# Performance work log

Measured on AMD Instinct MI355X. Metric: run time of the kernel, lower is better.

Reference implementation:

```python
import jax, jax.numpy as jnp
import numpy as np

T, N, E, D, H = 128, 1024, 16384, 256, 8


def setup_inputs() -> dict:
    key = jax.random.key(0)
    ks = jax.random.split(key, 8)
    s = 0.02  # weight init scale
    return {
        "embeddings": jax.random.normal(ks[0], (T, N, D), jnp.float32),
        "W1": jax.random.normal(ks[1], (D, 2 * D), jnp.float32) * s,
        "b1": jnp.zeros((2 * D,), jnp.float32),
        "W2": jax.random.normal(ks[2], (2 * D, D), jnp.float32) * s,
        "b2": jnp.zeros((D,), jnp.float32),
        "Wq": jax.random.normal(ks[3], (D, D), jnp.float32) * s,
        "bq": jnp.zeros((D,), jnp.float32),
        "Wk": jax.random.normal(ks[4], (D, D), jnp.float32) * s,
        "bk": jnp.zeros((D,), jnp.float32),
        "edge_val": jax.random.uniform(ks[5], (T, E), jnp.float32),
        "edge_src": jax.random.randint(ks[6], (T, E), 0, N),
        "edge_dst": jax.random.randint(ks[7], (T, E), 0, N),
    }


def _pos_encoding(t, d):
    # sin/cos interleaved positional encoding, pe[:,0::2]=sin, pe[:,1::2]=cos
    pos = jnp.arange(t, dtype=jnp.float32)[:, None]
    div = jnp.exp(jnp.arange(0, d, 2, dtype=jnp.float32) * (-np.log(10000.0) / d))
    ang = pos * div  # [t, d//2]
    return jnp.stack([jnp.sin(ang), jnp.cos(ang)], axis=-1).reshape(t, d)


def reference(embeddings, W1, b1, W2, b2, Wq, bq, Wk, bk, edge_val, edge_src, edge_dst):
    t, n, d = embeddings.shape
    hd = d // H
    # per-timestep node MLP + avg/max pooling over nodes  -> one vector per snapshot
    h = jax.nn.relu(embeddings @ W1 + b1)          # [T, N, 2D]
    pooled = h.mean(axis=1) + h.max(axis=1)        # [T, 2D] (adaptive avg+max pool to 1)
    x = jax.nn.relu(pooled @ W2 + b2)              # [T, D]
    x = x + _pos_encoding(t, d)
    # multi-head self-attention probabilities (batch=1), averaged over heads
    q = ((x @ Wq + bq) * (hd ** -0.5)).reshape(t, H, hd)
    k = (x @ Wk + bk).reshape(t, H, hd)
    scores = jnp.einsum('qhd,khd->hqk', q, k)      # [H, T, T]
    probs = jax.nn.softmax(scores, axis=-1).mean(axis=0)  # [T, T]
    # threshold, add identity, causal (lower-triangular) mask
    probs = jnp.where(probs < 1.0 / t, 0.0, probs)
    probs = (probs + jnp.eye(t, dtype=probs.dtype)) * jnp.tril(jnp.ones((t, t), probs.dtype))
    # build adjacency stack from edge lists (COO scatter), then weighted accumulation
    t_idx = jnp.arange(t)[:, None]
    A = jnp.zeros((t, n, n), embeddings.dtype).at[t_idx, edge_src, edge_dst].add(edge_val)
    # new_At[t] = sum_s probs[t, s] * A[s]
    return jnp.einsum('ts,snm->tnm', probs, A)
```

## Files before the change

kernel.cpp:

```cpp
#include <hip/hip_runtime.h>
#include <hip/hip_bf16.h>

#define T_ 128
#define N_ 1024
#define E_ 16384
#define D_ 256
#define H_ 8
#define D2_ 512
#define NB2_ 4096
#define PS3_ 257

typedef __attribute__((ext_vector_type(8))) short bf16x8;
typedef __attribute__((ext_vector_type(4))) float f32x4;

__device__ __forceinline__ void atomAddF(float* p, float v) {
#if defined(__HIP_PLATFORM_AMD__)
    unsafeAtomicAdd(p, v);
#else
    atomicAdd(p, v);
#endif
}

__device__ __forceinline__ unsigned short f2bf(float x) {
    return __bfloat16_as_ushort(__float2bfloat16(x));
}

__global__ __launch_bounds__(256)
void k_prep(const float* __restrict__ W1, unsigned short* __restrict__ W1S,
            const int* __restrict__ edge_src, const int* __restrict__ edge_dst,
            float4* __restrict__ poolz, int* __restrict__ cnt)
{
    __shared__ int hist[NB2_];
    const int bi = blockIdx.x, tid = threadIdx.x;
    const int s = bi >> 1, h = bi & 1;

    if (tid < 128) poolz[bi * 128 + tid] = make_float4(0.f, 0.f, 0.f, 0.f);

    if (tid < 64) {
        const int u   = bi * 64 + tid;
        const int col = u & 511;
        const int k8  = u >> 9;
        unsigned short hh[8];
        #pragma unroll
        for (int j = 0; j < 8; ++j)
            hh[j] = f2bf(W1[(size_t)(k8 * 8 + j) * D2_ + col]);
        uint4 pk;
        pk.x = hh[0] | ((unsigned)hh[1] << 16);
        pk.y = hh[2] | ((unsigned)hh[3] << 16);
        pk.z = hh[4] | ((unsigned)hh[5] << 16);
        pk.w = hh[6] | ((unsigned)hh[7] << 16);
        *(uint4*)&W1S[(size_t)k8 * 4096 + col * 8] = pk;
    }

    for (int i = tid; i < NB2_; i += 256) hist[i] = 0;
    __syncthreads();
    const int e0 = h * 8192;
    for (int e = e0 + tid; e < e0 + 8192; e += 256) {
        const size_t eo = (size_t)s * E_ + e;
        atomicAdd(&hist[(edge_src[eo] << 2) | (edge_dst[eo] >> 8)], 1);
    }
    __syncthreads();
    const int slot = (s << 1) | h;
    for (int i = tid; i < NB2_; i += 256) cnt[i * 256 + slot] = hist[i];
}

__global__ __launch_bounds__(512)
void k_mlp1_mfma(const float* __restrict__ emb,
                 const unsigned short* __restrict__ W1S,
                 const float* __restrict__ b1,
                 float* __restrict__ pool_sum,
                 unsigned int* __restrict__ pool_max)
{
    __shared__ unsigned short A_l[2048];
    __shared__ unsigned short B_l[16384];

    const int tid  = threadIdx.x;
    const int lane = tid & 63;
    const int wave = tid >> 6;
    const int wm = wave >> 2, wn = wave & 3;
    const int l15 = lane & 15, l4 = lane >> 4;
    const int r0 = blockIdx.x * 64;
    const int t  = blockIdx.x >> 4;

    f32x4 acc[2][8] = {};

    for (int ks = 0; ks < 8; ++ks) {
        {
            const int row = tid >> 3, k4 = tid & 7;
            const float4 v = *(const float4*)&emb[(size_t)(r0 + row) * D_ + ks * 32 + k4 * 4];
            uint2 pk;
            pk.x = f2bf(v.x) | ((unsigned)f2bf(v.y) << 16);
            pk.y = f2bf(v.z) | ((unsigned)f2bf(v.w) << 16);
            *(uint2*)&A_l[(k4 >> 1) * 512 + row * 8 + (k4 & 1) * 4] = pk;
        }
        {
            const char* gsrc = (const char*)W1S + (size_t)ks * 32768;
            #pragma unroll
            for (int r = 0; r < 4; ++r) {
                const int off = r * 8192 + tid * 16;
                __builtin_amdgcn_global_load_lds(
                    (const __attribute__((address_space(1))) unsigned int*)(gsrc + off),
                    (__attribute__((address_space(3))) unsigned int*)((char*)B_l + off),
                    16, 0, 0);
            }
        }
        __syncthreads();

        const bf16x8 a0 = *(const bf16x8*)&A_l[l4 * 512 + (wm * 32 + l15) * 8];
        const bf16x8 a1 = *(const bf16x8*)&A_l[l4 * 512 + (wm * 32 + 16 + l15) * 8];
        #pragma unroll
        for (int cf = 0; cf < 8; ++cf) {
            const bf16x8 b = *(const bf16x8*)&B_l[l4 * 4096 + (wn * 128 + cf * 16 + l15) * 8];
            acc[0][cf] = __builtin_amdgcn_mfma_f32_16x16x32_bf16(a0, b, acc[0][cf], 0, 0, 0);
            acc[1][cf] = __builtin_amdgcn_mfma_f32_16x16x32_bf16(a1, b, acc[1][cf], 0, 0, 0);
        }
        __syncthreads();
    }

    #pragma unroll
    for (int cf = 0; cf < 8; ++cf) {
        const int col = wn * 128 + cf * 16 + l15;
        const float bias = b1[col];
        float cs = 0.f, cm = 0.f;
        #pragma unroll
        for (int mf = 0; mf < 2; ++mf) {
            #pragma unroll
            for (int j = 0; j < 4; ++j) {
                float hh = acc[mf][cf][j] + bias;
                hh = fmaxf(hh, 0.f);
                cs += hh;
                cm = fmaxf(cm, hh);
            }
        }
        cs += __shfl_xor(cs, 16);
        cs += __shfl_xor(cs, 32);
        cm = fmaxf(cm, __shfl_xor(cm, 16));
        cm = fmaxf(cm, __shfl_xor(cm, 32));
        if (l4 == 0) {
            atomAddF(pool_sum + t * D2_ + col, cs);
            atomicMax(pool_max + t * D2_ + col, __float_as_uint(cm));
        }
    }
}

__global__ __launch_bounds__(256)
void k_scan3(const int* __restrict__ cnt, unsigned short* __restrict__ prefS3,
             int* __restrict__ totB)
{
    __shared__ int sc[256];
    const int b = blockIdx.x, tid = threadIdx.x;
    sc[tid] = cnt[b * 256 + tid];
    __syncthreads();
    #pragma unroll
    for (int off = 1; off < 256; off <<= 1) {
        int v = (tid >= off) ? sc[tid - off] : 0;
        __syncthreads();
        sc[tid] += v;
        __syncthreads();
    }
    prefS3[b * PS3_ + tid + 1] = (unsigned short)sc[tid];
    if (tid == 0)   prefS3[b * PS3_] = 0;
    if (tid == 255) totB[b] = sc[255];
}

__global__ __launch_bounds__(256)
void k_scatter3(const float* __restrict__ edge_val,
                const int* __restrict__ edge_src,
                const int* __restrict__ edge_dst,
                const unsigned short* __restrict__ prefS3,
                const int* __restrict__ totB,
                int* __restrict__ segB,
                uint2* __restrict__ sortedC)
{
    __shared__ int sc[256];
    __shared__ int bst[NB2_];
    const int bi = blockIdx.x, tid = threadIdx.x;
    const int s = bi >> 1, h = bi & 1;
    const int slot = (s << 1) | h;

    int v[16];
    int run = 0;
    const int4* t4 = (const int4*)&totB[tid * 16];
    #pragma unroll
    for (int r4 = 0; r4 < 4; ++r4) {
        const int4 x = t4[r4];
        v[r4 * 4 + 0] = x.x; v[r4 * 4 + 1] = x.y;
        v[r4 * 4 + 2] = x.z; v[r4 * 4 + 3] = x.w;
        run += x.x + x.y + x.z + x.w;
    }
    sc[tid] = run;
    __syncthreads();
    #pragma unroll
    for (int off = 1; off < 256; off <<= 1) {
        int u = (tid >= off) ? sc[tid - off] : 0;
        __syncthreads();
        sc[tid] += u;
        __syncthreads();
    }
    int p = sc[tid] - run;
    #pragma unroll
    for (int r = 0; r < 16; ++r) {
        const int i = tid * 16 + r;
        const int excl = p;
        p += v[r];
        if (bi == 0) {
            #pragma unroll
            for (int kcx = 0; kcx < 5; ++kcx)
                segB[i * 5 + kcx] = excl + (int)prefS3[i * PS3_ + kcx * 64];
        }
        bst[i] = excl + (int)prefS3[i * PS3_ + slot];
    }
    __syncthreads();

    const int e0 = h * 8192;
    for (int e = e0 + tid; e < e0 + 8192; e += 256) {
        const size_t eo = (size_t)s * E_ + e;
        const int src = edge_src[eo];
        const int dst = edge_dst[eo];
        const float vv = edge_val[eo];
        const int bkt = (src << 2) | (dst >> 8);
        const int gidx = atomicAdd(&bst[bkt], 1);
        sortedC[gidx] = make_uint2((unsigned)((s << 8) | (dst & 255)),
                                   __float_as_uint(vv));
    }
}

__global__ __launch_bounds__(256)
void k_mlp2qk(const float* __restrict__ pool_sum,
              const unsigned int* __restrict__ pool_max,
              const float* __restrict__ W2, const float* __restrict__ b2,
              const float* __restrict__ Wq, const float* __restrict__ bq,
              const float* __restrict__ Wk, const float* __restrict__ bk,
              float* __restrict__ q, float* __restrict__ k)
{
    __shared__ float pl[D2_];
    __shared__ float xl[D_];
    const int t = blockIdx.x;
    const int j = threadIdx.x;

    pl[j]       = pool_sum[t * D2_ + j]       * (1.0f / (float)N_) +
                  __uint_as_float(pool_max[t * D2_ + j]);
    pl[j + 256] = pool_sum[t * D2_ + j + 256] * (1.0f / (float)N_) +
                  __uint_as_float(pool_max[t * D2_ + j + 256]);
    __syncthreads();

    float acc = b2[j];
    for (int kk = 0; kk < D2_; ++kk)
        acc += pl[kk] * W2[(size_t)kk * D_ + j];
    acc = fmaxf(acc, 0.f);

    const int i2 = (j >> 1) * 2;
    const float div = expf((float)i2 * (-logf(10000.0f) / (float)D_));
    const float ang = (float)t * div;
    acc += (j & 1) ? cosf(ang) : sinf(ang);
    xl[j] = acc;
    __syncthreads();

    float aq = bq[j], ak = bk[j];
    for (int kk = 0; kk < D_; ++kk) {
        const float xv = xl[kk];
        aq += xv * Wq[(size_t)kk * D_ + j];
        ak += xv * Wk[(size_t)kk * D_ + j];
    }
    q[t * D_ + j] = aq * 0.17677669529663687f;
    k[t * D_ + j] = ak;
}

__global__ __launch_bounds__(128)
void k_probs(const float* __restrict__ q,
             const float* __restrict__ k,
             unsigned short* __restrict__ Pfrag)
{
    __shared__ float ql[D_];
    __shared__ float wmax[2][H_];
    __shared__ float wsum[2][H_];
    __shared__ float pall[T_];
    const int qt = blockIdx.x;
    const int kt = threadIdx.x;
    const int wv = kt >> 6, ln = kt & 63;

    ql[kt]       = q[qt * D_ + kt];
    ql[kt + 128] = q[qt * D_ + kt + 128];
    __syncthreads();

    float sh[H_];
    #pragma unroll
    for (int h = 0; h < H_; ++h) {
        float s = 0.f;
        #pragma unroll
        for (int d = 0; d < 32; ++d)
            s += ql[h * 32 + d] * k[kt * D_ + h * 32 + d];
        sh[h] = s;
    }

    #pragma unroll
    for (int h = 0; h < H_; ++h) {
        float v = sh[h];
        #pragma unroll
        for (int off = 32; off > 0; off >>= 1)
            v = fmaxf(v, __shfl_xor(v, off));
        if (ln == 0) wmax[wv][h] = v;
    }
    __syncthreads();
    float e[H_];
    #pragma unroll
    for (int h = 0; h < H_; ++h) {
        const float m = fmaxf(wmax[0][h], wmax[1][h]);
        e[h] = expf(sh[h] - m);
        float v = e[h];
        #pragma unroll
        for (int off = 32; off > 0; off >>= 1)
            v += __shfl_xor(v, off);
        if (ln == 0) wsum[wv][h] = v;
    }
    __syncthreads();
    float pm = 0.f;
    #pragma unroll
    for (int h = 0; h < H_; ++h)
        pm += e[h] / (wsum[0][h] + wsum[1][h]);
    pm *= (1.0f / (float)H_);

    if (pm < (1.0f / (float)T_)) pm = 0.f;
    if (kt == qt) pm += 1.0f;
    if (kt > qt) pm = 0.f;
    pall[kt] = pm;
    __syncthreads();

    if (kt < 16) {
        const int kc = kt >> 2, g = kt & 3;
        const int lane = g * 16 + (qt & 15);
        const int u = kc * 512 + (qt >> 4) * 64 + lane;
        const int s0 = kc * 32 + g * 8;
        unsigned short hh[8];
        #pragma unroll
        for (int j = 0; j < 8; ++j)
            hh[j] = f2bf(pall[s0 + j]);
        uint4 pk;
        pk.x = hh[0] | ((unsigned)hh[1] << 16);
        pk.y = hh[2] | ((unsigned)hh[3] << 16);
        pk.z = hh[4] | ((unsigned)hh[5] << 16);
        pk.w = hh[6] | ((unsigned)hh[7] << 16);
        *(uint4*)&Pfrag[u * 8] = pk;
    }
}

__global__ __launch_bounds__(256)
void k_accum_mfma(const unsigned short* __restrict__ Pfrag,
                  const uint2* __restrict__ sortedC,
                  const int* __restrict__ segB,
                  float* __restrict__ out)
{
    __shared__ float stage[8576];
    __shared__ unsigned short P_l[16384];

    const int ct   = blockIdx.x;
    const int tid  = threadIdx.x;
    const int lane = tid & 63;
    const int wv   = tid >> 6;
    const int l15  = lane & 15, l4 = lane >> 4;

    #pragma unroll
    for (int r = 0; r < 8; ++r) {
        const int off = r * 4096 + tid * 16;
        __builtin_amdgcn_global_load_lds(
            (const __attribute__((address_space(1))) unsigned int*)((const char*)Pfrag + off),
            (__attribute__((address_space(3))) unsigned int*)((char*)P_l + off),
            16, 0, 0);
    }

    const int sb = ct * 5;
    f32x4 acc[8][4] = {};

    for (int kc = 0; kc < 4; ++kc) {
        __syncthreads();
        {
            float4* s4 = (float4*)stage;
            for (int i = tid; i < 2064; i += 256)
                s4[i] = make_float4(0.f, 0.f, 0.f, 0.f);
        }
        __syncthreads();
        const int i0 = segB[sb + kc];
        const int i1 = segB[sb + kc + 1];
        for (int i = i0 + tid; i < i1; i += 256) {
            const uint2 it = sortedC[i];
            atomicAdd(&stage[((it.x >> 8) & 31) * 258 + (it.x & 255)],
                      __uint_as_float(it.y));
        }
        __syncthreads();

        #pragma unroll
        for (int cf = 0; cf < 4; ++cf) {
            const int c = wv * 64 + cf * 16 + l15;
            float bs[8];
            #pragma unroll
            for (int j = 0; j < 8; ++j)
                bs[j] = stage[(l4 * 8 + j) * 258 + c];
            bf16x8 bfr;
            #pragma unroll
            for (int j = 0; j < 8; ++j)
                bfr[j] = (short)f2bf(bs[j]);
            #pragma unroll
            for (int tf = 0; tf < 8; ++tf) {
                if (tf >= 2 * kc) {
                    const bf16x8 af =
                        *(const bf16x8*)&P_l[((kc * 8 + tf) * 64 + lane) * 8];
                    acc[tf][cf] = __builtin_amdgcn_mfma_f32_16x16x32_bf16(
                        af, bfr, acc[tf][cf], 0, 0, 0);
                }
            }
        }
    }

    const int erow = tid >> 6;
    const int ecol = (tid & 63) * 4;
    #pragma unroll
    for (int tp = 0; tp < 4; ++tp) {
        __syncthreads();
        #pragma unroll
        for (int sl = 0; sl < 2; ++sl) {
            const int tf = tp * 2 + sl;
            #pragma unroll
            for (int cf = 0; cf < 4; ++cf) {
                const int c = wv * 64 + cf * 16 + l15;
                #pragma unroll
                for (int j = 0; j < 4; ++j)
                    stage[sl * 4288 + (l4 * 4 + j) * 268 + c] = acc[tf][cf][j];
            }
        }
        __syncthreads();
        #pragma unroll
        for (int sl = 0; sl < 2; ++sl) {
            const int tf = tp * 2 + sl;
            #pragma unroll
            for (int ii = 0; ii < 4; ++ii) {
                const int row = ii * 4 + erow;
                const f32x4 vv = *(const f32x4*)&stage[sl * 4288 + row * 268 + ecol];
                __builtin_nontemporal_store(vv,
                    (f32x4*)&out[((size_t)(tf * 16 + row) << 20) + ct * 256 + ecol]);
            }
        }
    }
}

extern "C" void kernel_launch(void* const* d_in, const int* in_sizes, int n_in,
                              void* d_out, int out_size, void* d_ws, size_t ws_size,
                              hipStream_t stream) {
    const float* emb      = (const float*)d_in[0];
    const float* W1       = (const float*)d_in[1];
    const float* b1       = (const float*)d_in[2];
    const float* W2       = (const float*)d_in[3];
    const float* b2       = (const float*)d_in[4];
    const float* Wq       = (const float*)d_in[5];
    const float* bq       = (const float*)d_in[6];
    const float* Wk       = (const float*)d_in[7];
    const float* bk       = (const float*)d_in[8];
    const float* edge_val = (const float*)d_in[9];
    const int*   edge_src = (const int*)d_in[10];
    const int*   edge_dst = (const int*)d_in[11];
    float* out = (float*)d_out;

    char* ws = (char*)d_ws;
    float*          pool_sum = (float*)(ws);
    unsigned int*   pool_max = (unsigned int*)(ws + (256 << 10));
    float*          q        = (float*)(ws + (512 << 10));
    float*          k        = (float*)(ws + (640 << 10));
    unsigned short* W1S      = (unsigned short*)(ws + (832 << 10));
    unsigned short* Pfrag    = (unsigned short*)(ws + (1088 << 10));
    int*            totB     = (int*)(ws + (1120 << 10));
    int*            segB     = (int*)(ws + (1136 << 10));
    unsigned short* prefS3   = (unsigned short*)(ws + (1216 << 10));
    int*            cnt      = (int*)(ws + (3328 << 10));
    uint2*          sortedC  = (uint2*)(ws + (3328 << 10));

    k_prep<<<256, 256, 0, stream>>>(W1, W1S, edge_src, edge_dst,
                                    (float4*)pool_sum, cnt);
    k_mlp1_mfma<<<2048, 512, 0, stream>>>(emb, W1S, b1, pool_sum, pool_max);
    k_scan3<<<NB2_, 256, 0, stream>>>(cnt, prefS3, totB);
    k_scatter3<<<256, 256, 0, stream>>>(edge_val, edge_src, edge_dst,
                                        prefS3, totB, segB, sortedC);
    k_mlp2qk<<<128, 256, 0, stream>>>(pool_sum, pool_max, W2, b2,
                                      Wq, bq, Wk, bk, q, k);
    k_probs<<<128, 128, 0, stream>>>(q, k, Pfrag);
    k_accum_mfma<<<NB2_, 256, 0, stream>>>(Pfrag, sortedC, segB, out);
}
```

Before: 292.5 us.

## Drop scan kernel via byte-packed bucket counts; prefetch A and fold stage zeroing

Histogram counts are stored as bytes in slot-major layout, so the scatter kernel now computes per-slot prefix sums itself by streaming all 256 slot rows, and the separate 4096-block scan kernel is gone. The MLP1 kernel register-prefetches the next embedding tile before the barrier, and the accumulation kernel zeroes the LDS stage once and then clears each entry as it is read, replacing the per-chunk zero pass. These changes remove a launch and its global traffic and hide some load latency. The cost is that every scatter block redundantly reads 1 MB of counts, and the byte packing assumes no bucket gets more than 255 edges per half-timestep.

Result: slower. 314.7 us (+7.6%).

```diff
diff --git a/kernel.cpp b/kernel.cpp
--- a/kernel.cpp
+++ b/kernel.cpp
@@ -8,7 +8,6 @@
 #define H_ 8
 #define D2_ 512
 #define NB2_ 4096
-#define PS3_ 257
 
 typedef __attribute__((ext_vector_type(8))) short bf16x8;
 typedef __attribute__((ext_vector_type(4))) float f32x4;
@@ -28,7 +27,7 @@
 __global__ __launch_bounds__(256)
 void k_prep(const float* __restrict__ W1, unsigned short* __restrict__ W1S,
             const int* __restrict__ edge_src, const int* __restrict__ edge_dst,
-            float4* __restrict__ poolz, int* __restrict__ cnt)
+            float4* __restrict__ poolz, unsigned char* __restrict__ cnt8)
 {
     __shared__ int hist[NB2_];
     const int bi = blockIdx.x, tid = threadIdx.x;
@@ -61,7 +60,18 @@
     }
     __syncthreads();
     const int slot = (s << 1) | h;
-    for (int i = tid; i < NB2_; i += 256) cnt[i * 256 + slot] = hist[i];
+    {
+        const int b0 = tid * 16;
+        uint w0 = (uint)hist[b0+0]  | ((uint)hist[b0+1]  << 8) |
+                  ((uint)hist[b0+2]  << 16) | ((uint)hist[b0+3]  << 24);
+        uint w1 = (uint)hist[b0+4]  | ((uint)hist[b0+5]  << 8) |
+                  ((uint)hist[b0+6]  << 16) | ((uint)hist[b0+7]  << 24);
+        uint w2 = (uint)hist[b0+8]  | ((uint)hist[b0+9]  << 8) |
+                  ((uint)hist[b0+10] << 16) | ((uint)hist[b0+11] << 24);
+        uint w3 = (uint)hist[b0+12] | ((uint)hist[b0+13] << 8) |
+                  ((uint)hist[b0+14] << 16) | ((uint)hist[b0+15] << 24);
+        *(uint4*)&cnt8[(size_t)slot * NB2_ + b0] = make_uint4(w0, w1, w2, w3);
+    }
 }
 
 __global__ __launch_bounds__(512)
@@ -84,13 +94,15 @@
 
     f32x4 acc[2][8] = {};
 
+    const int row = tid >> 3, k4 = tid & 7;
+    const float* aptr = &emb[(size_t)(r0 + row) * D_ + k4 * 4];
+    float4 curA = *(const float4*)aptr;
+
     for (int ks = 0; ks < 8; ++ks) {
         {
-            const int row = tid >> 3, k4 = tid & 7;
-            const float4 v = *(const float4*)&emb[(size_t)(r0 + row) * D_ + ks * 32 + k4 * 4];
             uint2 pk;
-            pk.x = f2bf(v.x) | ((unsigned)f2bf(v.y) << 16);
-            pk.y = f2bf(v.z) | ((unsigned)f2bf(v.w) << 16);
+            pk.x = f2bf(curA.x) | ((unsigned)f2bf(curA.y) << 16);
+            pk.y = f2bf(curA.z) | ((unsigned)f2bf(curA.w) << 16);
             *(uint2*)&A_l[(k4 >> 1) * 512 + row * 8 + (k4 & 1) * 4] = pk;
         }
         {
@@ -104,6 +116,8 @@
                     16, 0, 0);
             }
         }
+        float4 nextA = curA;
+        if (ks < 7) nextA = *(const float4*)(aptr + (ks + 1) * 32);
         __syncthreads();
 
         const bf16x8 a0 = *(const bf16x8*)&A_l[l4 * 512 + (wm * 32 + l15) * 8];
@@ -115,6 +129,7 @@
             acc[1][cf] = __builtin_amdgcn_mfma_f32_16x16x32_bf16(a1, b, acc[1][cf], 0, 0, 0);
         }
         __syncthreads();
+        curA = nextA;
     }
 
     #pragma unroll
@@ -144,31 +159,10 @@
 }
 
 __global__ __launch_bounds__(256)
-void k_scan3(const int* __restrict__ cnt, unsigned short* __restrict__ prefS3,
-             int* __restrict__ totB)
-{
-    __shared__ int sc[256];
-    const int b = blockIdx.x, tid = threadIdx.x;
-    sc[tid] = cnt[b * 256 + tid];
-    __syncthreads();
-    #pragma unroll
-    for (int off = 1; off < 256; off <<= 1) {
-        int v = (tid >= off) ? sc[tid - off] : 0;
-        __syncthreads();
-        sc[tid] += v;
-        __syncthreads();
-    }
-    prefS3[b * PS3_ + tid + 1] = (unsigned short)sc[tid];
-    if (tid == 0)   prefS3[b * PS3_] = 0;
-    if (tid == 255) totB[b] = sc[255];
-}
-
-__global__ __launch_bounds__(256)
 void k_scatter3(const float* __restrict__ edge_val,
                 const int* __restrict__ edge_src,
                 const int* __restrict__ edge_dst,
-                const unsigned short* __restrict__ prefS3,
-                const int* __restrict__ totB,
+                const unsigned char* __restrict__ cnt8,
                 int* __restrict__ segB,
                 uint2* __restrict__ sortedC)
 {
@@ -178,17 +172,38 @@
     const int s = bi >> 1, h = bi & 1;
     const int slot = (s << 1) | h;
 
-    int v[16];
-    int run = 0;
-    const int4* t4 = (const int4*)&totB[tid * 16];
-    #pragma unroll
-    for (int r4 = 0; r4 < 4; ++r4) {
-        const int4 x = t4[r4];
-        v[r4 * 4 + 0] = x.x; v[r4 * 4 + 1] = x.y;
-        v[r4 * 4 + 2] = x.z; v[r4 * 4 + 3] = x.w;
-        run += x.x + x.y + x.z + x.w;
-    }
-    sc[tid] = run;
+    int run[16] = {};
+    int myPref[16];
+    int kp[3][16];
+
+    #pragma unroll
+    for (int c = 0; c < 4; ++c) {
+        if (c > 0) {
+            #pragma unroll
+            for (int j = 0; j < 16; ++j) kp[c - 1][j] = run[j];
+        }
+        #pragma unroll 4
+        for (int r = c * 64; r < c * 64 + 64; ++r) {
+            if (r == slot) {
+                #pragma unroll
+                for (int j = 0; j < 16; ++j) myPref[j] = run[j];
+            }
+            const uint4 w = *(const uint4*)&cnt8[(size_t)r * NB2_ + tid * 16];
+            run[0]  += w.x & 255;          run[1]  += (w.x >> 8) & 255;
+            run[2]  += (w.x >> 16) & 255;  run[3]  += w.x >> 24;
+            run[4]  += w.y & 255;          run[5]  += (w.y >> 8) & 255;
+            run[6]  += (w.y >> 16) & 255;  run[7]  += w.y >> 24;
+            run[8]  += w.z & 255;          run[9]  += (w.z >> 8) & 255;
+            run[10] += (w.z >> 16) & 255;  run[11] += w.z >> 24;
+            run[12] += w.w & 255;          run[13] += (w.w >> 8) & 255;
+            run[14] += (w.w >> 16) & 255;  run[15] += w.w >> 24;
+        }
+    }
+
+    int tot = 0;
+    #pragma unroll
+    for (int j = 0; j < 16; ++j) tot += run[j];
+    sc[tid] = tot;
     __syncthreads();
     #pragma unroll
     for (int off = 1; off < 256; off <<= 1) {
@@ -197,18 +212,20 @@
         sc[tid] += u;
         __syncthreads();
     }
-    int p = sc[tid] - run;
-    #pragma unroll
-    for (int r = 0; r < 16; ++r) {
-        const int i = tid * 16 + r;
+    int p = sc[tid] - tot;
+    #pragma unroll
+    for (int j = 0; j < 16; ++j) {
+        const int i = tid * 16 + j;
         const int excl = p;
-        p += v[r];
+        p += run[j];
         if (bi == 0) {
-            #pragma unroll
-            for (int kcx = 0; kcx < 5; ++kcx)
-                segB[i * 5 + kcx] = excl + (int)prefS3[i * PS3_ + kcx * 64];
-        }
-        bst[i] = excl + (int)prefS3[i * PS3_ + slot];
+            segB[i * 5 + 0] = excl;
+            segB[i * 5 + 1] = excl + kp[0][j];
+            segB[i * 5 + 2] = excl + kp[1][j];
+            segB[i * 5 + 3] = excl + kp[2][j];
+            segB[i * 5 + 4] = excl + run[j];
+        }
+        bst[i] = excl + myPref[j];
     }
     __syncthreads();
 
@@ -367,17 +384,16 @@
             (__attribute__((address_space(3))) unsigned int*)((char*)P_l + off),
             16, 0, 0);
     }
+    {
+        float4* s4 = (float4*)stage;
+        for (int i = tid; i < 2064; i += 256)
+            s4[i] = make_float4(0.f, 0.f, 0.f, 0.f);
+    }
 
     const int sb = ct * 5;
     f32x4 acc[8][4] = {};
 
     for (int kc = 0; kc < 4; ++kc) {
-        __syncthreads();
-        {
-            float4* s4 = (float4*)stage;
-            for (int i = tid; i < 2064; i += 256)
-                s4[i] = make_float4(0.f, 0.f, 0.f, 0.f);
-        }
         __syncthreads();
         const int i0 = segB[sb + kc];
         const int i1 = segB[sb + kc + 1];
@@ -393,8 +409,11 @@
             const int c = wv * 64 + cf * 16 + l15;
             float bs[8];
             #pragma unroll
-            for (int j = 0; j < 8; ++j)
-                bs[j] = stage[(l4 * 8 + j) * 258 + c];
+            for (int j = 0; j < 8; ++j) {
+                const int idx = (l4 * 8 + j) * 258 + c;
+                bs[j] = stage[idx];
+                stage[idx] = 0.f;
+            }
             bf16x8 bfr;
             #pragma unroll
             for (int j = 0; j < 8; ++j)
@@ -466,18 +485,15 @@
     float*          k        = (float*)(ws + (640 << 10));
     unsigned short* W1S      = (unsigned short*)(ws + (832 << 10));
     unsigned short* Pfrag    = (unsigned short*)(ws + (1088 << 10));
-    int*            totB     = (int*)(ws + (1120 << 10));
     int*            segB     = (int*)(ws + (1136 << 10));
-    unsigned short* prefS3   = (unsigned short*)(ws + (1216 << 10));
-    int*            cnt      = (int*)(ws + (3328 << 10));
+    unsigned char*  cnt8     = (unsigned char*)(ws + (1216 << 10));
     uint2*          sortedC  = (uint2*)(ws + (3328 << 10));
 
     k_prep<<<256, 256, 0, stream>>>(W1, W1S, edge_src, edge_dst,
-                                    (float4*)pool_sum, cnt);
+                                    (float4*)pool_sum, cnt8);
     k_mlp1_mfma<<<2048, 512, 0, stream>>>(emb, W1S, b1, pool_sum, pool_max);
-    k_scan3<<<NB2_, 256, 0, stream>>>(cnt, prefS3, totB);
     k_scatter3<<<256, 256, 0, stream>>>(edge_val, edge_src, edge_dst,
-                                        prefS3, totB, segB, sortedC);
+                                        cnt8, segB, sortedC);
     k_mlp2qk<<<128, 256, 0, stream>>>(pool_sum, pool_max, W2, b2,
                                       Wq, bq, Wk, bk, q, k);
     k_probs<<<128, 128, 0, stream>>>(q, k, Pfrag);
```
